# Performance work log

Hardware: AMD Instinct MI355X
Metric: run time of the kernel (lower is better)

## Reference

```python
import jax, jax.numpy as jnp
import numpy as np

B, N, C = 16, 577, 768
H = 12
HD = C // H            # 64 head dim
F = HD // 2            # 32 rotary frequency pairs
END = 24               # sqrt(N - 1): patch grid side
SCALE = HD ** -0.5


def setup_inputs() -> dict:
    key = jax.random.key(0)
    k0, k1, k2, k3 = jax.random.split(key, 4)
    x = jax.random.normal(k0, (B, N, C), jnp.float32)
    qkv_w = jax.random.normal(k1, (3 * C, C), jnp.float32) * 0.02
    proj_w = jax.random.normal(k2, (C, C), jnp.float32) * 0.02
    proj_b = jnp.zeros((C,), jnp.float32)
    # learnable mixed 2D RoPE frequencies, [2, H*F] as in init_2d_freqs().view(2,-1)
    freqs = jax.random.normal(k3, (2, H * F), jnp.float32) * 0.5
    return {"x": x, "qkv_w": qkv_w, "proj_w": proj_w, "proj_b": proj_b, "freqs": freqs}


def _rope_angles(freqs):
    # compute_mixed_cis: per-head angle = t_x*fx + t_y*fy over the 24x24 grid
    t = jnp.arange(END * END, dtype=jnp.float32)
    t_x = t % END
    t_y = jnp.floor(t / END)
    ang = t_x[:, None] * freqs[0][None, :] + t_y[:, None] * freqs[1][None, :]  # [Np, H*F]
    return ang.reshape(END * END, H, F).transpose(1, 0, 2)  # [H, Np, F]


def _apply_rope(q, cos, sin):
    # q: [B,H,Np,HD] viewed as complex pairs [B,H,Np,F,2]; rotate by e^{i*ang}
    qp = q.reshape(*q.shape[:-1], F, 2)
    re, im = qp[..., 0], qp[..., 1]
    out = jnp.stack([re * cos - im * sin, re * sin + im * cos], axis=-1)
    return out.reshape(q.shape)


def reference(x, qkv_w, proj_w, proj_b, freqs):
    qkv = (x @ qkv_w.T).reshape(B, N, 3, H, HD).transpose(2, 0, 3, 1, 4)
    q, k, v = qkv[0], qkv[1], qkv[2]              # each [B,H,N,HD]
    ang = _rope_angles(freqs)                      # [H, Np, F]
    cos = jnp.cos(ang)[None]                       # [1,H,Np,F]
    sin = jnp.sin(ang)[None]
    # CLS token (index 0) bypasses RoPE
    q = jnp.concatenate([q[:, :, :1], _apply_rope(q[:, :, 1:], cos, sin)], axis=2)
    k = jnp.concatenate([k[:, :, :1], _apply_rope(k[:, :, 1:], cos, sin)], axis=2)
    attn = jax.nn.softmax((q * SCALE) @ jnp.swapaxes(k, -2, -1), axis=-1)  # [B,H,N,N]
    out = (attn @ v).transpose(0, 2, 1, 3).reshape(B, N, C)
    return out @ proj_w.T + proj_b
```

## Files before the change

kernel.cpp:

```cpp
#include <hip/hip_runtime.h>


typedef __bf16 bf16;
typedef __bf16 bf16x4 __attribute__((ext_vector_type(4)));
typedef __bf16 bf16x8 __attribute__((ext_vector_type(8)));
typedef float f32x4 __attribute__((ext_vector_type(4)));

namespace {
constexpr int kC = 768;
constexpr int kNtok = 577;
constexpr int kM = 16 * kNtok;
constexpr int kMpad = 9344;
constexpr int kTok = 640;
constexpr int kBH = 192;
}

typedef __attribute__((address_space(3))) unsigned int as3_u32;
typedef __attribute__((address_space(1))) unsigned int as1_u32;
__device__ __forceinline__ void gl16(const bf16* g, bf16* l) {
  __builtin_amdgcn_global_load_lds((const as1_u32*)g, (as3_u32*)l, 16, 0, 0);
}

__device__ __forceinline__ int swz_lid(int hid, int nwg) {
  int q = nwg >> 3, r = nwg & 7;
  int x = hid & 7, y = hid >> 3;
  int base = (x < r) ? x * (q + 1) : r * (q + 1) + (x - r) * q;
  return base + y;
}

__global__ __launch_bounds__(256) void prep_kernel(
    const float* __restrict__ x, const float* __restrict__ qkv_w,
    const float* __restrict__ proj_w, const float* __restrict__ freqs,
    bf16* __restrict__ xb, bf16* __restrict__ wqb, bf16* __restrict__ pwb,
    float* __restrict__ cosT, float* __restrict__ sinT) {
  const int bidx = (int)blockIdx.x;
  const int tid = (int)threadIdx.x;
  if (bidx < 3504) {
    int idx = bidx * 256 + tid;
    int m = idx / 96, c8 = (idx % 96) * 8;
    bf16x8 o;
    if (m < kM) {
      const float* p = x + (size_t)m * kC + c8;
#pragma unroll
      for (int j = 0; j < 8; ++j) o[j] = (bf16)p[j];
    } else {
#pragma unroll
      for (int j = 0; j < 8; ++j) o[j] = (bf16)0.0f;
    }
    *(bf16x8*)(xb + (size_t)m * kC + c8) = o;
  } else if (bidx < 3504 + 864) {
    int off = ((bidx - 3504) * 256 + tid) * 8;
    bf16x8 o;
#pragma unroll
    for (int j = 0; j < 8; ++j) o[j] = (bf16)qkv_w[off + j];
    *(bf16x8*)(wqb + off) = o;
  } else if (bidx < 3504 + 864 + 288) {
    int off = ((bidx - 3504 - 864) * 256 + tid) * 8;
    bf16x8 o;
#pragma unroll
    for (int j = 0; j < 8; ++j) o[j] = (bf16)proj_w[off + j];
    *(bf16x8*)(pwb + off) = o;
  } else {
    int idx = (bidx - 3504 - 864 - 288) * 256 + tid;
    int f = idx & 31;
    int t = (idx >> 5) % 576;
    int h = idx / (576 * 32);
    float ang = (float)(t % 24) * freqs[h * 32 + f] + (float)(t / 24) * freqs[384 + h * 32 + f];
    float s, c;
    sincosf(ang, &s, &c);
    cosT[idx] = c;
    sinT[idx] = s;
  }
}

__global__ __launch_bounds__(512, 4) void qkv_gemm_kernel(
    const bf16* __restrict__ xb, const bf16* __restrict__ wb,
    const float* __restrict__ cosT, const float* __restrict__ sinT,
    bf16* __restrict__ qh, bf16* __restrict__ kbq, bf16* __restrict__ vb) {
  __shared__ __align__(16) char smem[65536];
  bf16* AsB = (bf16*)smem;
  bf16* BsB = (bf16*)(smem + 32768);
  const int tid = (int)threadIdx.x;
  const int l = tid & 63, w = tid >> 6;
  const int lr = l & 15, lg = l >> 4;
  const int wr = (w & 3) * 32, wc = (w >> 2) * 64;

  const int lid = swz_lid((int)blockIdx.x, 18 * 73);
  const int n0 = (lid % 18) * 128, m0 = (lid / 18) * 128;

  const int srow = w * 16 + (l >> 3);
  const int gch = (l & 7) ^ ((l >> 3) & 7);
  const bf16* aG = xb + (size_t)(m0 + srow) * kC + gch * 8;
  const bf16* bG = wb + (size_t)(n0 + srow) * kC + gch * 8;

  f32x4 acc[2][4];
  const f32x4 z = {0.f, 0.f, 0.f, 0.f};
#pragma unroll
  for (int mi = 0; mi < 2; ++mi)
#pragma unroll
    for (int ni = 0; ni < 4; ++ni) acc[mi][ni] = z;

  auto STAGE = [&](int buf, int k0) {
#pragma unroll
    for (int i = 0; i < 2; ++i) {
      gl16(aG + (size_t)i * 8 * kC + k0, &AsB[buf * 8192 + (w * 16 + i * 8) * 64]);
      gl16(bG + (size_t)i * 8 * kC + k0, &BsB[buf * 8192 + (w * 16 + i * 8) * 64]);
    }
  };
  auto COMPUTE = [&](int buf) {
    __builtin_amdgcn_s_setprio(1);
#pragma unroll
    for (int kc = 0; kc < 2; ++kc) {
      bf16x8 af[2], bfr[4];
#pragma unroll
      for (int ni = 0; ni < 4; ++ni) {
        int row = wc + ni * 16 + lr;
        bfr[ni] = *(const bf16x8*)&BsB[buf * 8192 + row * 64 + (((kc * 4 + lg) ^ (lr & 7)) << 3)];
      }
#pragma unroll
      for (int mi = 0; mi < 2; ++mi) {
        int row = wr + mi * 16 + lr;
        af[mi] = *(const bf16x8*)&AsB[buf * 8192 + row * 64 + (((kc * 4 + lg) ^ (lr & 7)) << 3)];
      }
#pragma unroll
      for (int mi = 0; mi < 2; ++mi)
#pragma unroll
        for (int ni = 0; ni < 4; ++ni)
          acc[mi][ni] = __builtin_amdgcn_mfma_f32_16x16x32_bf16(af[mi], bfr[ni], acc[mi][ni], 0, 0, 0);
    }
    __builtin_amdgcn_s_setprio(0);
  };

  STAGE(0, 0);
#pragma unroll 1
  for (int t = 0; t < 11; ++t) {
    const int buf = t & 1;
    STAGE(buf ^ 1, (t + 1) * 64);
    asm volatile("s_waitcnt vmcnt(4)" ::: "memory");
    __builtin_amdgcn_sched_barrier(0);
    __builtin_amdgcn_s_barrier();
    COMPUTE(buf);
    __builtin_amdgcn_s_barrier();
    __builtin_amdgcn_sched_barrier(0);
  }
  asm volatile("s_waitcnt vmcnt(0)" ::: "memory");
  __builtin_amdgcn_sched_barrier(0);
  __builtin_amdgcn_s_barrier();
  COMPUTE(1);

  __syncthreads();
  float* tp = (float*)smem + w * 2048;
#pragma unroll
  for (int mi = 0; mi < 2; ++mi)
#pragma unroll
    for (int ni = 0; ni < 4; ++ni)
#pragma unroll
      for (int r = 0; r < 4; ++r)
        tp[(mi * 16 + lg * 4 + r) * 64 + ni * 16 + lr] = acc[mi][ni][r];

  const int which = n0 / kC;
  const int h = ((n0 + wc) % kC) >> 6;
  bf16* dst = (which == 0) ? qh : (which == 1) ? kbq : vb;
  const float sc = (which == 0) ? 0.125f : 1.0f;
  const int c4 = lr * 4;
#pragma unroll
  for (int i = 0; i < 8; ++i) {
    const int row = i * 4 + lg;
    const int m = m0 + wr + row;
    if (m >= kM) continue;
    float4 v4 = *(const float4*)&tp[row * 64 + c4];
    const int b = m / kNtok;
    const int tok = m - b * kNtok;
    float e0 = v4.x, o0 = v4.y, e1 = v4.z, o1 = v4.w;
    if (which < 2 && tok > 0) {
      const int tb = (h * 576 + tok - 1) * 32 + (c4 >> 1);
      float2 cc = *(const float2*)&cosT[tb];
      float2 ss = *(const float2*)&sinT[tb];
      float r0 = e0 * cc.x - o0 * ss.x, i0 = e0 * ss.x + o0 * cc.x;
      float r1 = e1 * cc.y - o1 * ss.y, i1 = e1 * ss.y + o1 * cc.y;
      e0 = r0; o0 = i0; e1 = r1; o1 = i1;
    }
    bf16x4 ov;
    ov[0] = (bf16)(e0 * sc); ov[1] = (bf16)(o0 * sc);
    ov[2] = (bf16)(e1 * sc); ov[3] = (bf16)(o1 * sc);
    *(bf16x4*)(dst + (((size_t)(b * 12 + h)) * kTok + tok) * 64 + c4) = ov;
  }
}

__global__ __launch_bounds__(256) void vtrans_kernel(const bf16* __restrict__ vb,
                                                     bf16* __restrict__ vtb) {
  __shared__ __align__(16) bf16 T[64][72];
  const int bh = (int)blockIdx.x, s = (int)blockIdx.y;
  const int t = (int)threadIdx.x;
  const int row = t >> 2, qr = t & 3;
  const int tok = s * 64 + row;
  bf16x8 v0, v1;
  if (tok < kNtok) {
    const bf16* p = vb + ((size_t)bh * kTok + tok) * 64 + qr * 16;
    v0 = *(const bf16x8*)p;
    v1 = *(const bf16x8*)(p + 8);
  } else {
#pragma unroll
    for (int j = 0; j < 8; ++j) { v0[j] = (bf16)0.0f; v1[j] = (bf16)0.0f; }
  }
#pragma unroll
  for (int j = 0; j < 8; ++j) {
    T[qr * 16 + j][row] = v0[j];
    T[qr * 16 + 8 + j][row] = v1[j];
  }
  __syncthreads();
  const int d = row;
  bf16x8 o0 = *(const bf16x8*)&T[d][qr * 16];
  bf16x8 o1 = *(const bf16x8*)&T[d][qr * 16 + 8];
  bf16* dst = vtb + ((size_t)bh * 64 + d) * kTok + s * 64 + qr * 16;
  *(bf16x8*)dst = o0;
  *(bf16x8*)(dst + 8) = o1;
}

__global__ __launch_bounds__(512, 8) void attn_kernel(
    const bf16* __restrict__ qh, const bf16* __restrict__ kbq, const bf16* __restrict__ vtb,
    bf16* __restrict__ aoh) {
  __shared__ __align__(16) bf16 Ks[2][64 * 64];
  __shared__ __align__(16) bf16 Vs[2][64 * 64];
  __shared__ __align__(16) bf16 Ps[8][16 * 64];
  const int tid = (int)threadIdx.x;
  const int l = tid & 63, w = tid >> 6;
  const int lr = l & 15, lg = l >> 4;

  const int lid = swz_lid((int)blockIdx.x, 5 * kBH);
  const int bh = lid / 5, qt = lid - bh * 5;
  const int q0 = qt * 128;

  const int srow = w * 8 + (l >> 3);
  const int gch = (l & 7) ^ ((l >> 3) & 7);
  const bf16* kG = kbq + ((size_t)bh * kTok + srow) * 64 + gch * 8;
  const bf16* vG = vtb + ((size_t)bh * 64 + srow) * kTok + gch * 8;

  auto STAGE = [&](int buf, int j0) {
    gl16(kG + (size_t)j0 * 64, &Ks[buf][(w * 8) * 64]);
    gl16(vG + j0, &Vs[buf][(w * 8) * 64]);
  };

  bf16x8 qf[2];
  {
    const bf16* qp = qh + ((size_t)bh * kTok + (q0 + w * 16 + lr)) * 64 + lg * 8;
    qf[0] = *(const bf16x8*)qp;
    qf[1] = *(const bf16x8*)(qp + 32);
  }
  bf16x8 ones;
#pragma unroll
  for (int j = 0; j < 8; ++j) ones[j] = (bf16)1.0f;

  const f32x4 z = {0.f, 0.f, 0.f, 0.f};
  f32x4 o[4];
#pragma unroll
  for (int nf = 0; nf < 4; ++nf) o[nf] = z;
  f32x4 den = z;

  STAGE(0, 0);
#pragma unroll 1
  for (int jt = 0; jt < 9; ++jt) {
    const int cur = jt & 1;
    __syncthreads();
    if (jt < 8) STAGE(cur ^ 1, (jt + 1) * 64);

    f32x4 s[4];
#pragma unroll
    for (int ni = 0; ni < 4; ++ni) s[ni] = z;
    __builtin_amdgcn_s_setprio(1);
#pragma unroll
    for (int kc = 0; kc < 2; ++kc) {
#pragma unroll
      for (int ni = 0; ni < 4; ++ni) {
        int row = ni * 16 + lr;
        bf16x8 kf = *(const bf16x8*)&Ks[cur][row * 64 + (((kc * 4 + lg) ^ (row & 7)) << 3)];
        s[ni] = __builtin_amdgcn_mfma_f32_16x16x32_bf16(qf[kc], kf, s[ni], 0, 0, 0);
      }
    }
    __builtin_amdgcn_s_setprio(0);

#pragma unroll
    for (int ni = 0; ni < 4; ++ni)
#pragma unroll
      for (int r = 0; r < 4; ++r) {
        float p = __expf(s[ni][r]);
        int prow = lg * 4 + r;
        int pcol = ni * 16 + lr;
        Ps[w][prow * 64 + ((((pcol >> 3) ^ (prow & 7)) & 7) << 3) + (pcol & 7)] = (bf16)p;
      }

    __builtin_amdgcn_s_setprio(1);
#pragma unroll
    for (int kc = 0; kc < 2; ++kc) {
      bf16x8 pf = *(const bf16x8*)&Ps[w][lr * 64 + (((kc * 4 + lg) ^ (lr & 7)) << 3)];
      den = __builtin_amdgcn_mfma_f32_16x16x32_bf16(pf, ones, den, 0, 0, 0);
#pragma unroll
      for (int nf = 0; nf < 4; ++nf) {
        int row = nf * 16 + lr;
        bf16x8 vf = *(const bf16x8*)&Vs[cur][row * 64 + (((kc * 4 + lg) ^ (row & 7)) << 3)];
        o[nf] = __builtin_amdgcn_mfma_f32_16x16x32_bf16(pf, vf, o[nf], 0, 0, 0);
      }
    }
    __builtin_amdgcn_s_setprio(0);
  }

  {
    const bf16* k576 = kbq + ((size_t)bh * kTok + 576) * 64;
    bf16x8 ka = *(const bf16x8*)(k576 + lg * 8);
    bf16x8 kb2 = *(const bf16x8*)(k576 + 32 + lg * 8);
    float part = 0.f;
#pragma unroll
    for (int j = 0; j < 8; ++j)
      part += (float)qf[0][j] * (float)ka[j] + (float)qf[1][j] * (float)kb2[j];
    part += __shfl_xor(part, 16);
    part += __shfl_xor(part, 32);
    float v576[4];
#pragma unroll
    for (int nf = 0; nf < 4; ++nf)
      v576[nf] = (float)vtb[((size_t)bh * 64 + nf * 16 + lr) * kTok + 576];
#pragma unroll
    for (int r = 0; r < 4; ++r) {
      float p = __expf(__shfl(part, lg * 4 + r));
      den[r] += p;
#pragma unroll
      for (int nf = 0; nf < 4; ++nf) o[nf][r] += p * v576[nf];
    }
  }

  const int b = bh / 12, h = bh % 12;
#pragma unroll
  for (int r = 0; r < 4; ++r) {
    const int tok = q0 + w * 16 + lg * 4 + r;
    if (tok > 576) continue;
    const float inv = 1.0f / den[r];
    const size_t rowb = ((size_t)(b * kNtok + tok)) * kC + h * 64;
#pragma unroll
    for (int nf = 0; nf < 4; ++nf)
      aoh[rowb + nf * 16 + lr] = (bf16)(o[nf][r] * inv);
  }
}

__global__ __launch_bounds__(512, 4) void proj_gemm_kernel(
    const bf16* __restrict__ ah, const bf16* __restrict__ bw,
    const float* __restrict__ bias, float* __restrict__ out) {
  __shared__ __align__(16) char smem[65536];
  bf16* AsB = (bf16*)smem;
  bf16* BsB = (bf16*)(smem + 32768);
  const int tid = (int)threadIdx.x;
  const int l = tid & 63, w = tid >> 6;
  const int lr = l & 15, lg = l >> 4;
  const int wr = (w & 3) * 32, wc = (w >> 2) * 64;

  const int lid = swz_lid((int)blockIdx.x, 6 * 73);
  const int n0 = (lid % 6) * 128, m0 = (lid / 6) * 128;

  const int srow = w * 16 + (l >> 3);
  const int gch = (l & 7) ^ ((l >> 3) & 7);
  const bf16* aG = ah + (size_t)(m0 + srow) * kC + gch * 8;
  const bf16* bG = bw + (size_t)(n0 + srow) * kC + gch * 8;

  f32x4 acc[2][4];
  const f32x4 z = {0.f, 0.f, 0.f, 0.f};
#pragma unroll
  for (int mi = 0; mi < 2; ++mi)
#pragma unroll
    for (int ni = 0; ni < 4; ++ni) acc[mi][ni] = z;

  auto STAGE = [&](int buf, int k0) {
#pragma unroll
    for (int i = 0; i < 2; ++i) {
      gl16(aG + (size_t)i * 8 * kC + k0, &AsB[buf * 8192 + (w * 16 + i * 8) * 64]);
      gl16(bG + (size_t)i * 8 * kC + k0, &BsB[buf * 8192 + (w * 16 + i * 8) * 64]);
    }
  };
  auto COMPUTE = [&](int buf) {
    __builtin_amdgcn_s_setprio(1);
#pragma unroll
    for (int kc = 0; kc < 2; ++kc) {
      bf16x8 af[2], bfr[4];
#pragma unroll
      for (int ni = 0; ni < 4; ++ni) {
        int row = wc + ni * 16 + lr;
        bfr[ni] = *(const bf16x8*)&BsB[buf * 8192 + row * 64 + (((kc * 4 + lg) ^ (lr & 7)) << 3)];
      }
#pragma unroll
      for (int mi = 0; mi < 2; ++mi) {
        int row = wr + mi * 16 + lr;
        af[mi] = *(const bf16x8*)&AsB[buf * 8192 + row * 64 + (((kc * 4 + lg) ^ (lr & 7)) << 3)];
      }
#pragma unroll
      for (int mi = 0; mi < 2; ++mi)
#pragma unroll
        for (int ni = 0; ni < 4; ++ni)
          acc[mi][ni] = __builtin_amdgcn_mfma_f32_16x16x32_bf16(af[mi], bfr[ni], acc[mi][ni], 0, 0, 0);
    }
    __builtin_amdgcn_s_setprio(0);
  };

  STAGE(0, 0);
#pragma unroll 1
  for (int t = 0; t < 11; ++t) {
    const int buf = t & 1;
    STAGE(buf ^ 1, (t + 1) * 64);
    asm volatile("s_waitcnt vmcnt(4)" ::: "memory");
    __builtin_amdgcn_sched_barrier(0);
    __builtin_amdgcn_s_barrier();
    COMPUTE(buf);
    __builtin_amdgcn_s_barrier();
    __builtin_amdgcn_sched_barrier(0);
  }
  asm volatile("s_waitcnt vmcnt(0)" ::: "memory");
  __builtin_amdgcn_sched_barrier(0);
  __builtin_amdgcn_s_barrier();
  COMPUTE(1);

  __syncthreads();
  float* tp = (float*)smem + w * 2048;
#pragma unroll
  for (int mi = 0; mi < 2; ++mi)
#pragma unroll
    for (int ni = 0; ni < 4; ++ni)
#pragma unroll
      for (int r = 0; r < 4; ++r)
        tp[(mi * 16 + lg * 4 + r) * 64 + ni * 16 + lr] = acc[mi][ni][r];

  const int c4 = lr * 4;
  const int ncol = n0 + wc + c4;
  float4 bv = *(const float4*)&bias[ncol];
#pragma unroll
  for (int i = 0; i < 8; ++i) {
    const int row = i * 4 + lg;
    const int m = m0 + wr + row;
    if (m >= kM) continue;
    float4 v4 = *(const float4*)&tp[row * 64 + c4];
    v4.x += bv.x; v4.y += bv.y; v4.z += bv.z; v4.w += bv.w;
    *(float4*)(out + (size_t)m * kC + ncol) = v4;
  }
}

extern "C" void kernel_launch(void* const* d_in, const int* in_sizes, int n_in,
                              void* d_out, int out_size, void* d_ws, size_t ws_size,
                              hipStream_t stream) {
  const float* x = (const float*)d_in[0];
  const float* qkv_w = (const float*)d_in[1];
  const float* proj_w = (const float*)d_in[2];
  const float* proj_b = (const float*)d_in[3];
  const float* freqs = (const float*)d_in[4];
  float* out = (float*)d_out;

  char* p = (char*)d_ws;
  auto take = [&](size_t bytes) { char* r = p; p += (bytes + 255) & ~(size_t)255; return r; };
  float* cosT = (float*)take(221184 * 4);
  float* sinT = (float*)take(221184 * 4);
  bf16* xb   = (bf16*)take((size_t)kMpad * kC * 2);
  bf16* wqb  = (bf16*)take((size_t)2304 * kC * 2);
  bf16* pwb  = (bf16*)take((size_t)kC * kC * 2);
  bf16* qh   = (bf16*)take((size_t)kBH * kTok * 64 * 2);
  bf16* kbq  = (bf16*)take((size_t)kBH * kTok * 64 * 2);
  bf16* vb   = (bf16*)take((size_t)kBH * kTok * 64 * 2);
  bf16* vtb  = (bf16*)take((size_t)kBH * 64 * kTok * 2);
  bf16* aoh  = (bf16*)take((size_t)kMpad * kC * 2);

  prep_kernel<<<3504 + 864 + 288 + 864, 256, 0, stream>>>(
      x, qkv_w, proj_w, freqs, xb, wqb, pwb, cosT, sinT);
  qkv_gemm_kernel<<<dim3(18 * 73), 512, 0, stream>>>(xb, wqb, cosT, sinT, qh, kbq, vb);
  vtrans_kernel<<<dim3(kBH, 10), 256, 0, stream>>>(vb, vtb);
  attn_kernel<<<dim3(5 * kBH), 512, 0, stream>>>(qh, kbq, vtb, aoh);
  proj_gemm_kernel<<<dim3(6 * 73), 512, 0, stream>>>(aoh, pwb, proj_b, out);
}
```

Measured before the change: 118.2 us.

## Enlarge QKV GEMM tiles to 256x256 with interleaved sub-tile load/compute schedule

The QKV projection GEMM moves from 128x128 tiles (1314 blocks) to 256x256 tiles (333 blocks) using 128KB of dynamic LDS. It adds a four-phase schedule inside each k-step that staggers the A/B half loads against MFMA quarters. The aim is more operand reuse per LDS byte and less global traffic. In exchange it cuts occupancy to 2 blocks per CU, raises register pressure with 32 accumulators per wave, and pads M to a multiple of 256, which gives poorer tail utilization on 256 CUs.

```diff
diff --git a/kernel.cpp b/kernel.cpp
--- a/kernel.cpp
+++ b/kernel.cpp
@@ -10,7 +10,7 @@
 constexpr int kC = 768;
 constexpr int kNtok = 577;
 constexpr int kM = 16 * kNtok;
-constexpr int kMpad = 9344;
+constexpr int kMpad = 9472;
 constexpr int kTok = 640;
 constexpr int kBH = 192;
 }
@@ -35,7 +35,7 @@
     float* __restrict__ cosT, float* __restrict__ sinT) {
   const int bidx = (int)blockIdx.x;
   const int tid = (int)threadIdx.x;
-  if (bidx < 3504) {
+  if (bidx < 3552) {
     int idx = bidx * 256 + tid;
     int m = idx / 96, c8 = (idx % 96) * 8;
     bf16x8 o;
@@ -48,20 +48,20 @@
       for (int j = 0; j < 8; ++j) o[j] = (bf16)0.0f;
     }
     *(bf16x8*)(xb + (size_t)m * kC + c8) = o;
-  } else if (bidx < 3504 + 864) {
-    int off = ((bidx - 3504) * 256 + tid) * 8;
+  } else if (bidx < 3552 + 864) {
+    int off = ((bidx - 3552) * 256 + tid) * 8;
     bf16x8 o;
 #pragma unroll
     for (int j = 0; j < 8; ++j) o[j] = (bf16)qkv_w[off + j];
     *(bf16x8*)(wqb + off) = o;
-  } else if (bidx < 3504 + 864 + 288) {
-    int off = ((bidx - 3504 - 864) * 256 + tid) * 8;
+  } else if (bidx < 3552 + 864 + 288) {
+    int off = ((bidx - 3552 - 864) * 256 + tid) * 8;
     bf16x8 o;
 #pragma unroll
     for (int j = 0; j < 8; ++j) o[j] = (bf16)proj_w[off + j];
     *(bf16x8*)(pwb + off) = o;
   } else {
-    int idx = (bidx - 3504 - 864 - 288) * 256 + tid;
+    int idx = (bidx - 3552 - 864 - 288) * 256 + tid;
     int f = idx & 31;
     int t = (idx >> 5) % 576;
     int h = idx / (576 * 32);
@@ -73,117 +73,151 @@
   }
 }
 
-__global__ __launch_bounds__(512, 4) void qkv_gemm_kernel(
+__global__ __launch_bounds__(512, 2) void qkv_gemm_kernel(
     const bf16* __restrict__ xb, const bf16* __restrict__ wb,
     const float* __restrict__ cosT, const float* __restrict__ sinT,
     bf16* __restrict__ qh, bf16* __restrict__ kbq, bf16* __restrict__ vb) {
-  __shared__ __align__(16) char smem[65536];
-  bf16* AsB = (bf16*)smem;
-  bf16* BsB = (bf16*)(smem + 32768);
+  extern __shared__ __align__(16) char smem[];
   const int tid = (int)threadIdx.x;
   const int l = tid & 63, w = tid >> 6;
   const int lr = l & 15, lg = l >> 4;
-  const int wr = (w & 3) * 32, wc = (w >> 2) * 64;
-
-  const int lid = swz_lid((int)blockIdx.x, 18 * 73);
-  const int n0 = (lid % 18) * 128, m0 = (lid / 18) * 128;
-
-  const int srow = w * 16 + (l >> 3);
+  const int wm = w >> 2, wn = w & 3;
+  const int w8 = w * 8;
+
+  const int lid = swz_lid((int)blockIdx.x, 37 * 9);
+  const int n0 = (lid % 9) * 256, m0 = (lid / 9) * 256;
+
   const int gch = (l & 7) ^ ((l >> 3) & 7);
-  const bf16* aG = xb + (size_t)(m0 + srow) * kC + gch * 8;
-  const bf16* bG = wb + (size_t)(n0 + srow) * kC + gch * 8;
-
-  f32x4 acc[2][4];
+  const bf16* aG = xb + (size_t)(m0 + w8 + (l >> 3)) * kC + gch * 8;
+  const bf16* bG = wb + (size_t)(n0 + w8 + (l >> 3)) * kC + gch * 8;
+
+  auto Abuf = [&](int b) { return (bf16*)(smem + b * 65536); };
+  auto Bbuf = [&](int b) { return (bf16*)(smem + b * 65536 + 32768); };
+
+  auto SA = [&](int b, int k0, int half) {
+    bf16* A = Abuf(b);
+    gl16(aG + (size_t)(half * 64) * kC + k0, A + (half * 64 + w8) * 64);
+    gl16(aG + (size_t)(half * 64 + 128) * kC + k0, A + (half * 64 + 128 + w8) * 64);
+  };
+  auto SB = [&](int b, int k0, int bh) {
+    bf16* B = Bbuf(b);
+    const int base = w8 + (w8 & 32) + bh * 32;
+    gl16(bG + (size_t)(base - w8) * kC + k0, B + base * 64);
+    gl16(bG + (size_t)(base - w8 + 128) * kC + k0, B + (base + 128) * 64);
+  };
+
+  f32x4 acc[8][4];
   const f32x4 z = {0.f, 0.f, 0.f, 0.f};
 #pragma unroll
-  for (int mi = 0; mi < 2; ++mi)
+  for (int mi = 0; mi < 8; ++mi)
 #pragma unroll
     for (int ni = 0; ni < 4; ++ni) acc[mi][ni] = z;
 
-  auto STAGE = [&](int buf, int k0) {
-#pragma unroll
-    for (int i = 0; i < 2; ++i) {
-      gl16(aG + (size_t)i * 8 * kC + k0, &AsB[buf * 8192 + (w * 16 + i * 8) * 64]);
-      gl16(bG + (size_t)i * 8 * kC + k0, &BsB[buf * 8192 + (w * 16 + i * 8) * 64]);
-    }
-  };
-  auto COMPUTE = [&](int buf) {
+  bf16x8 af[4][2], b0f[2][2], b1f[2][2];
+
+  auto RDA = [&](int b, int H) {
+    const bf16* A = Abuf(b);
+#pragma unroll
+    for (int mi = 0; mi < 4; ++mi) {
+      const int row = wm * 128 + (H * 4 + mi) * 16 + lr;
+#pragma unroll
+      for (int kc = 0; kc < 2; ++kc)
+        af[mi][kc] = *(const bf16x8*)&A[row * 64 + (((kc * 4 + lg) ^ (lr & 7)) << 3)];
+    }
+  };
+  auto RDB = [&](int b, int Bs, bf16x8 (*dst)[2]) {
+    const bf16* Bp = Bbuf(b);
+#pragma unroll
+    for (int nj = 0; nj < 2; ++nj) {
+      const int row = wn * 64 + (Bs * 2 + nj) * 16 + lr;
+#pragma unroll
+      for (int kc = 0; kc < 2; ++kc)
+        dst[nj][kc] = *(const bf16x8*)&Bp[row * 64 + (((kc * 4 + lg) ^ (lr & 7)) << 3)];
+    }
+  };
+  auto MM = [&](int H, int Bs, bf16x8 (*bq)[2]) {
     __builtin_amdgcn_s_setprio(1);
 #pragma unroll
-    for (int kc = 0; kc < 2; ++kc) {
-      bf16x8 af[2], bfr[4];
-#pragma unroll
-      for (int ni = 0; ni < 4; ++ni) {
-        int row = wc + ni * 16 + lr;
-        bfr[ni] = *(const bf16x8*)&BsB[buf * 8192 + row * 64 + (((kc * 4 + lg) ^ (lr & 7)) << 3)];
-      }
-#pragma unroll
-      for (int mi = 0; mi < 2; ++mi) {
-        int row = wr + mi * 16 + lr;
-        af[mi] = *(const bf16x8*)&AsB[buf * 8192 + row * 64 + (((kc * 4 + lg) ^ (lr & 7)) << 3)];
-      }
-#pragma unroll
-      for (int mi = 0; mi < 2; ++mi)
-#pragma unroll
-        for (int ni = 0; ni < 4; ++ni)
-          acc[mi][ni] = __builtin_amdgcn_mfma_f32_16x16x32_bf16(af[mi], bfr[ni], acc[mi][ni], 0, 0, 0);
-    }
+    for (int kc = 0; kc < 2; ++kc)
+#pragma unroll
+      for (int mi = 0; mi < 4; ++mi)
+#pragma unroll
+        for (int nj = 0; nj < 2; ++nj)
+          acc[H * 4 + mi][Bs * 2 + nj] = __builtin_amdgcn_mfma_f32_16x16x32_bf16(
+              af[mi][kc], bq[nj][kc], acc[H * 4 + mi][Bs * 2 + nj], 0, 0, 0);
     __builtin_amdgcn_s_setprio(0);
   };
-
-  STAGE(0, 0);
+  auto BAR = [&](int n) {
+    if (n == 0) asm volatile("s_waitcnt vmcnt(0)" ::: "memory");
+    else if (n == 2) asm volatile("s_waitcnt vmcnt(2)" ::: "memory");
+    else if (n == 4) asm volatile("s_waitcnt vmcnt(4)" ::: "memory");
+    __builtin_amdgcn_sched_barrier(0);
+    __builtin_amdgcn_s_barrier();
+    __builtin_amdgcn_sched_barrier(0);
+  };
+
+  SA(0, 0, 0);
+  SB(0, 0, 0);
+  SB(0, 0, 1);
+  SA(0, 0, 1);
+
 #pragma unroll 1
   for (int t = 0; t < 11; ++t) {
-    const int buf = t & 1;
-    STAGE(buf ^ 1, (t + 1) * 64);
-    asm volatile("s_waitcnt vmcnt(4)" ::: "memory");
-    __builtin_amdgcn_sched_barrier(0);
-    __builtin_amdgcn_s_barrier();
-    COMPUTE(buf);
-    __builtin_amdgcn_s_barrier();
-    __builtin_amdgcn_sched_barrier(0);
-  }
-  asm volatile("s_waitcnt vmcnt(0)" ::: "memory");
+    const int cb = t & 1, nb = cb ^ 1;
+    const int k1 = (t + 1) * 64;
+    BAR(4);  RDA(cb, 0); RDB(cb, 0, b0f); SA(nb, k1, 0); MM(0, 0, b0f);
+    BAR(4);  RDB(cb, 1, b1f);             SB(nb, k1, 0); MM(0, 1, b1f);
+    BAR(4);  RDA(cb, 1);                  SB(nb, k1, 1); MM(1, 1, b1f);
+    BAR(-1); RDB(cb, 0, b0f);             SA(nb, k1, 1); MM(1, 0, b0f);
+  }
+  {
+    const int cb = 1;
+    BAR(4);  RDA(cb, 0); RDB(cb, 0, b0f); MM(0, 0, b0f);
+    BAR(2);  RDB(cb, 1, b1f);             MM(0, 1, b1f);
+    BAR(0);  RDA(cb, 1);                  MM(1, 1, b1f);
+    BAR(-1); RDB(cb, 0, b0f);             MM(1, 0, b0f);
+  }
+
   __builtin_amdgcn_sched_barrier(0);
-  __builtin_amdgcn_s_barrier();
-  COMPUTE(1);
-
   __syncthreads();
-  float* tp = (float*)smem + w * 2048;
-#pragma unroll
-  for (int mi = 0; mi < 2; ++mi)
-#pragma unroll
-    for (int ni = 0; ni < 4; ++ni)
-#pragma unroll
-      for (int r = 0; r < 4; ++r)
-        tp[(mi * 16 + lg * 4 + r) * 64 + ni * 16 + lr] = acc[mi][ni][r];
-
-  const int which = n0 / kC;
-  const int h = ((n0 + wc) % kC) >> 6;
+  float* tp = (float*)smem + w * 4096;
+  const int nbase = n0 + wn * 64;
+  const int which = nbase / kC;
+  const int h = (nbase % kC) >> 6;
   bf16* dst = (which == 0) ? qh : (which == 1) ? kbq : vb;
   const float sc = (which == 0) ? 0.125f : 1.0f;
   const int c4 = lr * 4;
 #pragma unroll
-  for (int i = 0; i < 8; ++i) {
-    const int row = i * 4 + lg;
-    const int m = m0 + wr + row;
-    if (m >= kM) continue;
-    float4 v4 = *(const float4*)&tp[row * 64 + c4];
-    const int b = m / kNtok;
-    const int tok = m - b * kNtok;
-    float e0 = v4.x, o0 = v4.y, e1 = v4.z, o1 = v4.w;
-    if (which < 2 && tok > 0) {
-      const int tb = (h * 576 + tok - 1) * 32 + (c4 >> 1);
-      float2 cc = *(const float2*)&cosT[tb];
-      float2 ss = *(const float2*)&sinT[tb];
-      float r0 = e0 * cc.x - o0 * ss.x, i0 = e0 * ss.x + o0 * cc.x;
-      float r1 = e1 * cc.y - o1 * ss.y, i1 = e1 * ss.y + o1 * cc.y;
-      e0 = r0; o0 = i0; e1 = r1; o1 = i1;
-    }
-    bf16x4 ov;
-    ov[0] = (bf16)(e0 * sc); ov[1] = (bf16)(o0 * sc);
-    ov[2] = (bf16)(e1 * sc); ov[3] = (bf16)(o1 * sc);
-    *(bf16x4*)(dst + (((size_t)(b * 12 + h)) * kTok + tok) * 64 + c4) = ov;
+  for (int ch = 0; ch < 2; ++ch) {
+#pragma unroll
+    for (int mi = 0; mi < 4; ++mi)
+#pragma unroll
+      for (int ni = 0; ni < 4; ++ni)
+#pragma unroll
+        for (int r = 0; r < 4; ++r)
+          tp[(mi * 16 + lg * 4 + r) * 64 + ni * 16 + lr] = acc[ch * 4 + mi][ni][r];
+#pragma unroll
+    for (int i = 0; i < 16; ++i) {
+      const int row = i * 4 + lg;
+      const int m = m0 + wm * 128 + ch * 64 + row;
+      if (m >= kM) continue;
+      float4 v4 = *(const float4*)&tp[row * 64 + c4];
+      const int b = m / kNtok;
+      const int tok = m - b * kNtok;
+      float e0 = v4.x, o0 = v4.y, e1 = v4.z, o1 = v4.w;
+      if (which < 2 && tok > 0) {
+        const int tb = (h * 576 + tok - 1) * 32 + (c4 >> 1);
+        float2 cc = *(const float2*)&cosT[tb];
+        float2 ss = *(const float2*)&sinT[tb];
+        float r0 = e0 * cc.x - o0 * ss.x, i0 = e0 * ss.x + o0 * cc.x;
+        float r1 = e1 * cc.y - o1 * ss.y, i1 = e1 * ss.y + o1 * cc.y;
+        e0 = r0; o0 = i0; e1 = r1; o1 = i1;
+      }
+      bf16x4 ov;
+      ov[0] = (bf16)(e0 * sc); ov[1] = (bf16)(o0 * sc);
+      ov[2] = (bf16)(e1 * sc); ov[3] = (bf16)(o1 * sc);
+      *(bf16x4*)(dst + (((size_t)(b * 12 + h)) * kTok + tok) * 64 + c4) = ov;
+    }
   }
 }
 
@@ -448,6 +482,13 @@
   const float* freqs = (const float*)d_in[4];
   float* out = (float*)d_out;
 
+  static int qkv_smem_set = 0;
+  if (!qkv_smem_set) {
+    hipFuncSetAttribute((const void*)qkv_gemm_kernel,
+                        hipFuncAttributeMaxDynamicSharedMemorySize, 131072);
+    qkv_smem_set = 1;
+  }
+
   char* p = (char*)d_ws;
   auto take = [&](size_t bytes) { char* r = p; p += (bytes + 255) & ~(size_t)255; return r; };
   float* cosT = (float*)take(221184 * 4);
@@ -461,9 +502,9 @@
   bf16* vtb  = (bf16*)take((size_t)kBH * 64 * kTok * 2);
   bf16* aoh  = (bf16*)take((size_t)kMpad * kC * 2);
 
-  prep_kernel<<<3504 + 864 + 288 + 864, 256, 0, stream>>>(
+  prep_kernel<<<3552 + 864 + 288 + 864, 256, 0, stream>>>(
       x, qkv_w, proj_w, freqs, xb, wqb, pwb, cosT, sinT);
-  qkv_gemm_kernel<<<dim3(18 * 73), 512, 0, stream>>>(xb, wqb, cosT, sinT, qh, kbq, vb);
+  qkv_gemm_kernel<<<dim3(37 * 9), 512, 131072, stream>>>(xb, wqb, cosT, sinT, qh, kbq, vb);
   vtrans_kernel<<<dim3(kBH, 10), 256, 0, stream>>>(vb, vtb);
   attn_kernel<<<dim3(5 * kBH), 512, 0, stream>>>(qh, kbq, vtb, aoh);
   proj_gemm_kernel<<<dim3(6 * 73), 512, 0, stream>>>(aoh, pwb, proj_b, out);
```

New measurement: 133.3 us. 1.13x slower.

## Fuse V transpose into QKV GEMM epilogue and drop vtrans kernel

Applied to the files above, without the earlier changes.

The QKV GEMM epilogue now handles V tiles (which == 2) separately. It stages them as bf16 in a padded shared-memory tile and writes them directly in transposed [bh, d, tok] layout. This removes the separate vtrans kernel launch and the round trip of V through global memory. The transposed writes are scalar 2-byte stores, and the padding tokens past 577 in vtb are no longer zeroed, which could matter if the attention kernel reads them.

```diff
diff --git a/kernel.cpp b/kernel.cpp
--- a/kernel.cpp
+++ b/kernel.cpp
@@ -76,7 +76,7 @@
 __global__ __launch_bounds__(512, 4) void qkv_gemm_kernel(
     const bf16* __restrict__ xb, const bf16* __restrict__ wb,
     const float* __restrict__ cosT, const float* __restrict__ sinT,
-    bf16* __restrict__ qh, bf16* __restrict__ kbq, bf16* __restrict__ vb) {
+    bf16* __restrict__ qh, bf16* __restrict__ kbq, bf16* __restrict__ vtb) {
   __shared__ __align__(16) char smem[65536];
   bf16* AsB = (bf16*)smem;
   bf16* BsB = (bf16*)(smem + 32768);
@@ -149,72 +149,65 @@
   COMPUTE(1);
 
   __syncthreads();
-  float* tp = (float*)smem + w * 2048;
-#pragma unroll
-  for (int mi = 0; mi < 2; ++mi)
-#pragma unroll
-    for (int ni = 0; ni < 4; ++ni)
-#pragma unroll
-      for (int r = 0; r < 4; ++r)
-        tp[(mi * 16 + lg * 4 + r) * 64 + ni * 16 + lr] = acc[mi][ni][r];
-
   const int which = n0 / kC;
   const int h = ((n0 + wc) % kC) >> 6;
-  bf16* dst = (which == 0) ? qh : (which == 1) ? kbq : vb;
-  const float sc = (which == 0) ? 0.125f : 1.0f;
-  const int c4 = lr * 4;
-#pragma unroll
-  for (int i = 0; i < 8; ++i) {
-    const int row = i * 4 + lg;
-    const int m = m0 + wr + row;
-    if (m >= kM) continue;
-    float4 v4 = *(const float4*)&tp[row * 64 + c4];
-    const int b = m / kNtok;
-    const int tok = m - b * kNtok;
-    float e0 = v4.x, o0 = v4.y, e1 = v4.z, o1 = v4.w;
-    if (which < 2 && tok > 0) {
-      const int tb = (h * 576 + tok - 1) * 32 + (c4 >> 1);
-      float2 cc = *(const float2*)&cosT[tb];
-      float2 ss = *(const float2*)&sinT[tb];
-      float r0 = e0 * cc.x - o0 * ss.x, i0 = e0 * ss.x + o0 * cc.x;
-      float r1 = e1 * cc.y - o1 * ss.y, i1 = e1 * ss.y + o1 * cc.y;
-      e0 = r0; o0 = i0; e1 = r1; o1 = i1;
-    }
-    bf16x4 ov;
-    ov[0] = (bf16)(e0 * sc); ov[1] = (bf16)(o0 * sc);
-    ov[2] = (bf16)(e1 * sc); ov[3] = (bf16)(o1 * sc);
-    *(bf16x4*)(dst + (((size_t)(b * 12 + h)) * kTok + tok) * 64 + c4) = ov;
-  }
-}
-
-__global__ __launch_bounds__(256) void vtrans_kernel(const bf16* __restrict__ vb,
-                                                     bf16* __restrict__ vtb) {
-  __shared__ __align__(16) bf16 T[64][72];
-  const int bh = (int)blockIdx.x, s = (int)blockIdx.y;
-  const int t = (int)threadIdx.x;
-  const int row = t >> 2, qr = t & 3;
-  const int tok = s * 64 + row;
-  bf16x8 v0, v1;
-  if (tok < kNtok) {
-    const bf16* p = vb + ((size_t)bh * kTok + tok) * 64 + qr * 16;
-    v0 = *(const bf16x8*)p;
-    v1 = *(const bf16x8*)(p + 8);
+
+  if (which == 2) {
+    bf16* tq = (bf16*)smem + w * 4096;
+#pragma unroll
+    for (int mi = 0; mi < 2; ++mi)
+#pragma unroll
+      for (int ni = 0; ni < 4; ++ni)
+#pragma unroll
+        for (int r = 0; r < 4; ++r)
+          tq[(mi * 16 + lg * 4 + r) * 65 + ni * 16 + lr] = (bf16)acc[mi][ni][r];
+    const int tokrow = l & 31;
+    const int dhalf = l >> 5;
+    const int m = m0 + wr + tokrow;
+    if (m < kM) {
+      const int b = m / kNtok;
+      const int tok = m - b * kNtok;
+      bf16* vdst = vtb + ((size_t)(b * 12 + h) * 64 + dhalf) * kTok + tok;
+#pragma unroll
+      for (int it = 0; it < 32; ++it)
+        vdst[(size_t)(it * 2) * kTok] = tq[tokrow * 65 + it * 2 + dhalf];
+    }
   } else {
-#pragma unroll
-    for (int j = 0; j < 8; ++j) { v0[j] = (bf16)0.0f; v1[j] = (bf16)0.0f; }
-  }
-#pragma unroll
-  for (int j = 0; j < 8; ++j) {
-    T[qr * 16 + j][row] = v0[j];
-    T[qr * 16 + 8 + j][row] = v1[j];
-  }
-  __syncthreads();
-  const int d = row;
-  bf16x8 o0 = *(const bf16x8*)&T[d][qr * 16];
-  bf16x8 o1 = *(const bf16x8*)&T[d][qr * 16 + 8];
-  bf16* dst = vtb + ((size_t)bh * 64 + d) * kTok + s * 64 + qr * 16;
-  *(bf16x8*)dst = o0;
-  *(bf16x8*)(dst + 8) = o1;
+    float* tp = (float*)smem + w * 2048;
+#pragma unroll
+    for (int mi = 0; mi < 2; ++mi)
+#pragma unroll
+      for (int ni = 0; ni < 4; ++ni)
+#pragma unroll
+        for (int r = 0; r < 4; ++r)
+          tp[(mi * 16 + lg * 4 + r) * 64 + ni * 16 + lr] = acc[mi][ni][r];
+
+    bf16* dst = (which == 0) ? qh : kbq;
+    const float sc = (which == 0) ? 0.125f : 1.0f;
+    const int c4 = lr * 4;
+#pragma unroll
+    for (int i = 0; i < 8; ++i) {
+      const int row = i * 4 + lg;
+      const int m = m0 + wr + row;
+      if (m >= kM) continue;
+      float4 v4 = *(const float4*)&tp[row * 64 + c4];
+      const int b = m / kNtok;
+      const int tok = m - b * kNtok;
+      float e0 = v4.x, o0 = v4.y, e1 = v4.z, o1 = v4.w;
+      if (tok > 0) {
+        const int tb = (h * 576 + tok - 1) * 32 + (c4 >> 1);
+        float2 cc = *(const float2*)&cosT[tb];
+        float2 ss = *(const float2*)&sinT[tb];
+        float r0 = e0 * cc.x - o0 * ss.x, i0 = e0 * ss.x + o0 * cc.x;
+        float r1 = e1 * cc.y - o1 * ss.y, i1 = e1 * ss.y + o1 * cc.y;
+        e0 = r0; o0 = i0; e1 = r1; o1 = i1;
+      }
+      bf16x4 ov;
+      ov[0] = (bf16)(e0 * sc); ov[1] = (bf16)(o0 * sc);
+      ov[2] = (bf16)(e1 * sc); ov[3] = (bf16)(o1 * sc);
+      *(bf16x4*)(dst + (((size_t)(b * 12 + h)) * kTok + tok) * 64 + c4) = ov;
+    }
+  }
 }
 
 __global__ __launch_bounds__(512, 8) void attn_kernel(
@@ -457,14 +450,12 @@
   bf16* pwb  = (bf16*)take((size_t)kC * kC * 2);
   bf16* qh   = (bf16*)take((size_t)kBH * kTok * 64 * 2);
   bf16* kbq  = (bf16*)take((size_t)kBH * kTok * 64 * 2);
-  bf16* vb   = (bf16*)take((size_t)kBH * kTok * 64 * 2);
   bf16* vtb  = (bf16*)take((size_t)kBH * 64 * kTok * 2);
   bf16* aoh  = (bf16*)take((size_t)kMpad * kC * 2);
 
   prep_kernel<<<3504 + 864 + 288 + 864, 256, 0, stream>>>(
       x, qkv_w, proj_w, freqs, xb, wqb, pwb, cosT, sinT);
-  qkv_gemm_kernel<<<dim3(18 * 73), 512, 0, stream>>>(xb, wqb, cosT, sinT, qh, kbq, vb);
-  vtrans_kernel<<<dim3(kBH, 10), 256, 0, stream>>>(vb, vtb);
+  qkv_gemm_kernel<<<dim3(18 * 73), 512, 0, stream>>>(xb, wqb, cosT, sinT, qh, kbq, vtb);
   attn_kernel<<<dim3(5 * kBH), 512, 0, stream>>>(qh, kbq, vtb, aoh);
   proj_gemm_kernel<<<dim3(6 * 73), 512, 0, stream>>>(aoh, pwb, proj_b, out);
 }
```

New measurement: 111.1 us. 1.06x faster.
